# Kernel optimization log

Measured on AMD Instinct MI355X. Metric: run time of the kernel, lower is better.

## Reference

```python
import jax, jax.numpy as jnp
import numpy as np
import math

ROWS, COLS, N_NODES = 256, 1024, 500000


def setup_inputs() -> dict:
    key = jax.random.key(0)
    ks = jax.random.split(key, 16)
    stdv_row = 1.0 / math.sqrt(ROWS)
    u = lambda k, shape, s: jax.random.uniform(k, shape, jnp.float32, -s, s)
    return {
        "prev_Q": jax.random.normal(ks[0], (ROWS, COLS), jnp.float32),
        "prev_Z": jax.random.normal(ks[1], (N_NODES, ROWS), jnp.float32),
        "mask": jnp.zeros((N_NODES,), jnp.float32),
        "scorer": u(ks[2], (ROWS, 1), stdv_row),
        "W_u": u(ks[3], (ROWS, ROWS), stdv_row),
        "U_u": u(ks[4], (ROWS, ROWS), stdv_row),
        "b_u": jnp.zeros((ROWS, COLS), jnp.float32),
        "W_r": u(ks[5], (ROWS, ROWS), stdv_row),
        "U_r": u(ks[6], (ROWS, ROWS), stdv_row),
        "b_r": jnp.zeros((ROWS, COLS), jnp.float32),
        "W_h": u(ks[7], (ROWS, ROWS), stdv_row),
        "U_h": u(ks[8], (ROWS, ROWS), stdv_row),
        "b_h": jnp.zeros((ROWS, COLS), jnp.float32),
    }


def reference(prev_Q, prev_Z, mask, scorer, W_u, U_u, b_u, W_r, U_r, b_r, W_h, U_h, b_h):
    k = b_u.shape[1]  # cols == TopK k
    # --- TopK node selection (k <= num_nodes, no -inf masked scores) ---
    scores = (prev_Z @ scorer).ravel() / jnp.linalg.norm(scorer) + mask  # [N]
    vals, idx = jax.lax.top_k(scores, k)                                 # [k]
    # selected nodes scaled by tanh(score), then transposed -> [rows, k]
    z_topk = (prev_Z[idx] * jnp.tanh(vals)[:, None]).T
    # --- matrix GRU gates ---
    update = jax.nn.sigmoid(W_u @ z_topk + U_u @ prev_Q + b_u)
    reset = jax.nn.sigmoid(W_r @ z_topk + U_r @ prev_Q + b_r)
    h_cap = jax.nn.relu(W_h @ z_topk + U_h @ (reset * prev_Q) + b_h)
    new_Q = (1.0 - update) * prev_Q + update * h_cap
    return new_Q
```

## Files before the change

kernel.cpp:

```cpp
#include <hip/hip_runtime.h>
#include <hip/hip_bf16.h>

#define NN 500000

typedef short bf16x8 __attribute__((ext_vector_type(8)));
typedef float f32x4 __attribute__((ext_vector_type(4)));

__device__ __forceinline__ unsigned f2key(float f){
    unsigned u = __float_as_uint(f);
    return (u & 0x80000000u) ? ~u : (u | 0x80000000u);
}
__device__ __forceinline__ unsigned long long d2key(double d){
    unsigned long long u = (unsigned long long)__double_as_longlong(d);
    return (u & 0x8000000000000000ull) ? ~u : (u | 0x8000000000000000ull);
}
__device__ __forceinline__ double key2d(unsigned long long k){
    unsigned long long u = (k & 0x8000000000000000ull) ? (k & 0x7FFFFFFFFFFFFFFFull) : ~k;
    return __longlong_as_double((long long)u);
}
__device__ __forceinline__ float sigmoidf_(float x){
    return 1.0f / (1.0f + expf(-x));
}
__device__ __forceinline__ short f2bf(float x){
    __hip_bfloat16 h = __float2bfloat16(x);
    return *reinterpret_cast<short*>(&h);
}

__global__ __launch_bounds__(256) void score_kernel(
    const float4* __restrict__ Z4, const float* __restrict__ mask,
    const float* __restrict__ scorer, double* __restrict__ scores_d)
{
    __shared__ double nred[256];
    __shared__ double s_invn;
    int tid = threadIdx.x;
    {
        double v = (double)scorer[tid];
        nred[tid] = v * v;
        __syncthreads();
        for (int s = 128; s > 0; s >>= 1){
            if (tid < s) nred[tid] += nred[tid + s];
            __syncthreads();
        }
        if (tid == 0) s_invn = 1.0 / sqrt(nred[0]);
        __syncthreads();
    }
    double invn = s_invn;
    int sl = tid & 15;
    int grp = tid >> 4;
    int gid = blockIdx.x * 16 + grp;
    const float4* s4 = (const float4*)scorer;
    float4 s0 = s4[sl], s1 = s4[sl + 16], s2 = s4[sl + 32], s3 = s4[sl + 48];
    for (int r = gid; r < NN; r += 24576){
        const float4* zp = Z4 + (size_t)r * 64;
        float4 z0 = zp[sl], z1 = zp[sl + 16], z2 = zp[sl + 32], z3 = zp[sl + 48];
        double p0 = (double)z0.x * s0.x + (double)z0.y * s0.y + (double)z0.z * s0.z + (double)z0.w * s0.w;
        double p1 = (double)z1.x * s1.x + (double)z1.y * s1.y + (double)z1.z * s1.z + (double)z1.w * s1.w;
        double p2 = (double)z2.x * s2.x + (double)z2.y * s2.y + (double)z2.z * s2.z + (double)z2.w * s2.w;
        double p3 = (double)z3.x * s3.x + (double)z3.y * s3.y + (double)z3.z * s3.z + (double)z3.w * s3.w;
        double d = (p0 + p1) + (p2 + p3);
        d += __shfl_xor(d, 8, 16);
        d += __shfl_xor(d, 4, 16);
        d += __shfl_xor(d, 2, 16);
        d += __shfl_xor(d, 1, 16);
        if (sl == 0){
            scores_d[r] = d * invn + (double)mask[r];
        }
    }
}

__global__ __launch_bounds__(256) void hist_transpose_kernel(
    const double* __restrict__ scores_d, unsigned* __restrict__ hist,
    const float* __restrict__ prev_Q, float* __restrict__ Qt)
{
    __shared__ __attribute__((aligned(16))) char smem[16640];
    int tid = threadIdx.x;
    int b = blockIdx.x;
    if (b < 256){
        unsigned* h = (unsigned*)smem;
        for (int i = tid; i < 4096; i += 256) h[i] = 0u;
        __syncthreads();
        for (int i = b * 256 + tid; i < NN; i += 65536){
            double sd = scores_d[i];
            atomicAdd(&h[f2key((float)sd) >> 20], 1u);
        }
        __syncthreads();
        for (int i = tid; i < 4096; i += 256){
            unsigned c = h[i];
            if (c) atomicAdd(&hist[i], c);
        }
    } else {
        float (*tile)[65] = (float (*)[65])smem;
        int tb = b - 256;
        int n0 = (tb & 15) * 64, m0 = (tb >> 4) * 64;
        for (int rep = 0; rep < 16; ++rep){
            int lin = tid + rep * 256;
            int r = lin >> 6, c = lin & 63;
            tile[r][c] = prev_Q[(m0 + r) * 1024 + n0 + c];
        }
        __syncthreads();
        for (int rep = 0; rep < 16; ++rep){
            int lin = tid + rep * 256;
            int r = lin >> 6, c = lin & 63;
            Qt[(n0 + r) * 256 + m0 + c] = tile[c][r];
        }
    }
}

__global__ __launch_bounds__(256) void collect_kernel(
    const double* __restrict__ scores_d, const unsigned* __restrict__ hist,
    unsigned* __restrict__ meta,
    unsigned long long* __restrict__ ckey, unsigned* __restrict__ cidx)
{
    __shared__ unsigned hl[4096];
    __shared__ unsigned part[256];
    __shared__ unsigned s_thr;
    int tid = threadIdx.x;
    for (int i = tid; i < 4096; i += 256) hl[i] = hist[i];
    __syncthreads();
    int hi = 4096 - 16 * tid;
    unsigned s = 0;
    for (int bb = hi - 16; bb < hi; ++bb) s += hl[bb];
    part[tid] = s;
    __syncthreads();
    for (int off = 1; off < 256; off <<= 1){
        unsigned v = (tid >= off) ? part[tid - off] : 0u;
        __syncthreads();
        part[tid] += v;
        __syncthreads();
    }
    unsigned incl = part[tid];
    unsigned excl = incl - s;
    if (excl < 1024u && incl >= 1024u){
        unsigned c = excl;
        int bb;
        for (bb = hi - 1; bb >= hi - 16; --bb){
            c += hl[bb];
            if (c >= 1024u) break;
        }
        s_thr = ((unsigned)bb) << 20;
    }
    __syncthreads();
    unsigned thr = s_thr;
    int i = blockIdx.x * 256 + tid;
    if (i < NN){
        double sd = scores_d[i];
        if (f2key((float)sd) >= thr){
            unsigned p = atomicAdd(&meta[3], 1u);
            if (p < 4096u){ ckey[p] = d2key(sd); cidx[p] = (unsigned)i; }
        }
    }
}

__global__ __launch_bounds__(1024) void sort_emit_kernel(const unsigned long long* __restrict__ ckey,
                                                         const unsigned* __restrict__ cidx,
                                                         const unsigned* __restrict__ meta,
                                                         unsigned* __restrict__ sel_idx,
                                                         float* __restrict__ sel_t)
{
    __shared__ unsigned long long sk[4096];
    __shared__ unsigned si[4096];
    int t = threadIdx.x;
    unsigned n = meta[3];
    if (n > 4096u) n = 4096u;
    int m = 1024;
    while (m < (int)n) m <<= 1;
    for (int i = t; i < m; i += 1024){
        if (i < (int)n){ sk[i] = ckey[i]; si[i] = cidx[i]; }
        else           { sk[i] = 0ull;    si[i] = 0xFFFFFFFFu; }
    }
    __syncthreads();
    int m2 = m >> 1;
    for (int k = 2; k <= m; k <<= 1){
        for (int j = k >> 1; j > 0; j >>= 1){
            for (int p = t; p < m2; p += 1024){
                int i = ((p & ~(j - 1)) << 1) | (p & (j - 1));
                int ip = i | j;
                unsigned long long ka = sk[i], kb = sk[ip];
                unsigned ia = si[i], ib = si[ip];
                bool ab = (ka > kb) || (ka == kb && ia < ib);
                bool desc = ((i & k) == 0);
                bool sw = desc ? (!ab) : ab;
                if (sw){ sk[i] = kb; sk[ip] = ka; si[i] = ib; si[ip] = ia; }
            }
            __syncthreads();
        }
    }
    sel_idx[t] = si[t];
    sel_t[t] = tanhf((float)key2d(sk[t]));
}

__global__ void gather_kernel(const float4* __restrict__ Z4,
                              const unsigned* __restrict__ sel_idx,
                              const float* __restrict__ sel_t,
                              float4* __restrict__ Xc4)
{
    int lane = threadIdx.x & 63;
    int col = (blockIdx.x << 2) + (threadIdx.x >> 6);
    unsigned idx = sel_idx[col];
    float tv = sel_t[col];
    float4 z = Z4[(size_t)idx * 64 + lane];
    float4 o; o.x = z.x * tv; o.y = z.y * tv; o.z = z.z * tv; o.w = z.w * tv;
    Xc4[col * 64 + lane] = o;
}

__global__ __launch_bounds__(256) void gemm1_mfma(
    const float* __restrict__ Wu, const float* __restrict__ Uu, const float* __restrict__ bu,
    const float* __restrict__ Wr, const float* __restrict__ Ur, const float* __restrict__ br,
    const float* __restrict__ Wh, const float* __restrict__ bh,
    const float* __restrict__ Xc, const float* __restrict__ Qt, const float* __restrict__ Q,
    float* __restrict__ Umat, float* __restrict__ RQt, float* __restrict__ P3m)
{
    __shared__ short As[4096];
    __shared__ short Xs[4096];
    int g = blockIdx.z;
    int n0 = blockIdx.x * 64, m0 = blockIdx.y * 64;
    int tid = threadIdx.x;
    int l = tid & 63, w = tid >> 6;
    int q = l >> 4, c16 = l & 15;
    f32x4 acc[4];
    #pragma unroll
    for (int i = 0; i < 4; ++i) acc[i] = (f32x4){0.f, 0.f, 0.f, 0.f};
    const float* W0 = (g == 0) ? Wu : (g == 1) ? Wr : Wh;
    const float* W1 = (g == 0) ? Uu : (g == 1) ? Ur : Wh;
    int KMAX = (g == 2) ? 256 : 512;
    for (int k0 = 0; k0 < KMAX; k0 += 64){
        const float* Asrc = (k0 < 256) ? W0 : W1;
        const float* Xsrc = (k0 < 256) ? Xc : Qt;
        int koff = k0 & 255;
        #pragma unroll
        for (int i = 0; i < 4; ++i){
            int f = tid + (i << 8);
            int row = f >> 4, c = f & 15;
            float4 av = *(const float4*)&Asrc[(m0 + row) * 256 + koff + (c << 2)];
            float4 xv = *(const float4*)&Xsrc[(n0 + row) * 256 + koff + (c << 2)];
            int kb = (c << 3) ^ ((row & 7) << 4);
            short4 ah; ah.x = f2bf(av.x); ah.y = f2bf(av.y); ah.z = f2bf(av.z); ah.w = f2bf(av.w);
            short4 xh; xh.x = f2bf(xv.x); xh.y = f2bf(xv.y); xh.z = f2bf(xv.z); xh.w = f2bf(xv.w);
            *(short4*)((char*)As + row * 128 + kb) = ah;
            *(short4*)((char*)Xs + row * 128 + kb) = xh;
        }
        __syncthreads();
        int swz = (c16 & 7) << 4;
        bf16x8 a0 = *(const bf16x8*)((const char*)As + ((w << 4) + c16) * 128 + (((q << 4)     ) ^ swz));
        bf16x8 a1 = *(const bf16x8*)((const char*)As + ((w << 4) + c16) * 128 + ((64 + (q << 4)) ^ swz));
        #pragma unroll
        for (int nr = 0; nr < 4; ++nr){
            int xrow = (nr << 4) + c16;
            bf16x8 b0 = *(const bf16x8*)((const char*)Xs + xrow * 128 + (((q << 4)     ) ^ swz));
            bf16x8 b1 = *(const bf16x8*)((const char*)Xs + xrow * 128 + ((64 + (q << 4)) ^ swz));
            acc[nr] = __builtin_amdgcn_mfma_f32_16x16x32_bf16(a0, b0, acc[nr], 0, 0, 0);
            acc[nr] = __builtin_amdgcn_mfma_f32_16x16x32_bf16(a1, b1, acc[nr], 0, 0, 0);
        }
        __syncthreads();
    }
    int mrow = m0 + (w << 4) + (q << 2);
    if (g == 0){
        #pragma unroll
        for (int nr = 0; nr < 4; ++nr){
            int ncol = n0 + (nr << 4) + c16;
            #pragma unroll
            for (int r = 0; r < 4; ++r){
                int idx = (mrow + r) * 1024 + ncol;
                Umat[idx] = sigmoidf_(acc[nr][r] + bu[idx]);
            }
        }
    } else if (g == 1){
        #pragma unroll
        for (int nr = 0; nr < 4; ++nr){
            int ncol = n0 + (nr << 4) + c16;
            float4 o;
            float* op = (float*)&o;
            #pragma unroll
            for (int r = 0; r < 4; ++r){
                int idx = (mrow + r) * 1024 + ncol;
                op[r] = sigmoidf_(acc[nr][r] + br[idx]) * Q[idx];
            }
            *(float4*)&RQt[ncol * 256 + mrow] = o;
        }
    } else {
        #pragma unroll
        for (int nr = 0; nr < 4; ++nr){
            int ncol = n0 + (nr << 4) + c16;
            #pragma unroll
            for (int r = 0; r < 4; ++r){
                int idx = (mrow + r) * 1024 + ncol;
                P3m[idx] = acc[nr][r] + bh[idx];
            }
        }
    }
}

__global__ __launch_bounds__(256) void gemm2_mfma(
    const float* __restrict__ Uh, const float* __restrict__ RQt,
    const float* __restrict__ P3m, const float* __restrict__ Umat,
    const float* __restrict__ Q, float* __restrict__ out)
{
    __shared__ short As[4096];
    __shared__ short Xs[4096];
    int n0 = blockIdx.x * 64, m0 = blockIdx.y * 64;
    int tid = threadIdx.x;
    int l = tid & 63, w = tid >> 6;
    int q = l >> 4, c16 = l & 15;
    f32x4 acc[4];
    #pragma unroll
    for (int i = 0; i < 4; ++i) acc[i] = (f32x4){0.f, 0.f, 0.f, 0.f};
    for (int k0 = 0; k0 < 256; k0 += 64){
        #pragma unroll
        for (int i = 0; i < 4; ++i){
            int f = tid + (i << 8);
            int row = f >> 4, c = f & 15;
            float4 av = *(const float4*)&Uh[(m0 + row) * 256 + k0 + (c << 2)];
            float4 xv = *(const float4*)&RQt[(n0 + row) * 256 + k0 + (c << 2)];
            int kb = (c << 3) ^ ((row & 7) << 4);
            short4 ah; ah.x = f2bf(av.x); ah.y = f2bf(av.y); ah.z = f2bf(av.z); ah.w = f2bf(av.w);
            short4 xh; xh.x = f2bf(xv.x); xh.y = f2bf(xv.y); xh.z = f2bf(xv.z); xh.w = f2bf(xv.w);
            *(short4*)((char*)As + row * 128 + kb) = ah;
            *(short4*)((char*)Xs + row * 128 + kb) = xh;
        }
        __syncthreads();
        int swz = (c16 & 7) << 4;
        bf16x8 a0 = *(const bf16x8*)((const char*)As + ((w << 4) + c16) * 128 + (((q << 4)     ) ^ swz));
        bf16x8 a1 = *(const bf16x8*)((const char*)As + ((w << 4) + c16) * 128 + ((64 + (q << 4)) ^ swz));
        #pragma unroll
        for (int nr = 0; nr < 4; ++nr){
            int xrow = (nr << 4) + c16;
            bf16x8 b0 = *(const bf16x8*)((const char*)Xs + xrow * 128 + (((q << 4)     ) ^ swz));
            bf16x8 b1 = *(const bf16x8*)((const char*)Xs + xrow * 128 + ((64 + (q << 4)) ^ swz));
            acc[nr] = __builtin_amdgcn_mfma_f32_16x16x32_bf16(a0, b0, acc[nr], 0, 0, 0);
            acc[nr] = __builtin_amdgcn_mfma_f32_16x16x32_bf16(a1, b1, acc[nr], 0, 0, 0);
        }
        __syncthreads();
    }
    int mrow = m0 + (w << 4) + (q << 2);
    #pragma unroll
    for (int nr = 0; nr < 4; ++nr){
        int ncol = n0 + (nr << 4) + c16;
        #pragma unroll
        for (int r = 0; r < 4; ++r){
            int idx = (mrow + r) * 1024 + ncol;
            float h = fmaxf(acc[nr][r] + P3m[idx], 0.0f);
            float u = Umat[idx];
            float qv = Q[idx];
            out[idx] = (1.0f - u) * qv + u * h;
        }
    }
}

extern "C" void kernel_launch(void* const* d_in, const int* in_sizes, int n_in,
                              void* d_out, int out_size, void* d_ws, size_t ws_size,
                              hipStream_t stream)
{
    const float* prev_Q = (const float*)d_in[0];
    const float* prev_Z = (const float*)d_in[1];
    const float* mask   = (const float*)d_in[2];
    const float* scorer = (const float*)d_in[3];
    const float* W_u = (const float*)d_in[4];
    const float* U_u = (const float*)d_in[5];
    const float* b_u = (const float*)d_in[6];
    const float* W_r = (const float*)d_in[7];
    const float* U_r = (const float*)d_in[8];
    const float* b_r = (const float*)d_in[9];
    const float* W_h = (const float*)d_in[10];
    const float* U_h = (const float*)d_in[11];
    const float* b_h = (const float*)d_in[12];

    char* ws = (char*)d_ws;
    double*             scores_d = (double*)            (ws + 0);
    unsigned*           hist     = (unsigned*)          (ws + 4000256);
    unsigned*           meta     = (unsigned*)          (ws + 4016640);
    unsigned long long* ckey     = (unsigned long long*)(ws + 4016704);
    unsigned*           cidx     = (unsigned*)          (ws + 4049472);
    unsigned*           sel_idx  = (unsigned*)          (ws + 4065856);
    float*              sel_t    = (float*)             (ws + 4069952);
    float*              Xc       = (float*)             (ws + 4100096);
    float*              Qt       = (float*)             (ws + 5148672);
    float*              Umat     = (float*)             (ws + 6197248);
    float*              RQt      = (float*)             (ws + 7245824);
    float*              P3m      = (float*)             (ws + 8294400);

    hipMemsetAsync(ws + 4000256, 0, 16448, stream);

    hipLaunchKernelGGL(score_kernel, dim3(1536), dim3(256), 0, stream,
                       (const float4*)prev_Z, mask, scorer, scores_d);
    hipLaunchKernelGGL(hist_transpose_kernel, dim3(320), dim3(256), 0, stream,
                       scores_d, hist, prev_Q, Qt);
    hipLaunchKernelGGL(collect_kernel, dim3(1954), dim3(256), 0, stream,
                       scores_d, hist, meta, ckey, cidx);
    hipLaunchKernelGGL(sort_emit_kernel, dim3(1), dim3(1024), 0, stream,
                       ckey, cidx, meta, sel_idx, sel_t);
    hipLaunchKernelGGL(gather_kernel, dim3(256), dim3(256), 0, stream,
                       (const float4*)prev_Z, sel_idx, sel_t, (float4*)Xc);
    hipLaunchKernelGGL(gemm1_mfma, dim3(16, 4, 3), dim3(256), 0, stream,
                       W_u, U_u, b_u, W_r, U_r, b_r, W_h, b_h,
                       Xc, Qt, prev_Q, Umat, RQt, P3m);
    hipLaunchKernelGGL(gemm2_mfma, dim3(16, 4), dim3(256), 0, stream,
                       U_h, RQt, P3m, Umat, prev_Q, (float*)d_out);
}
```

Baseline: 199.0 us.

## Replace single-block bitonic sort with multi-block rank-by-counting selection

The single 1024-thread block that bitonic-sorted up to 4096 candidates is replaced by a rank kernel over 16 blocks. Each thread computes its candidate's rank by comparing against every other candidate in shared memory, then writes the candidate directly if its rank falls within the top 1024. This spreads the work across more compute units and avoids the many barrier-separated sort stages, at the cost of O(n^2) comparisons and each block redundantly loading all candidates into shared memory.

```diff
diff --git a/kernel.cpp b/kernel.cpp
--- a/kernel.cpp
+++ b/kernel.cpp
@@ -151,42 +151,41 @@
     }
 }
 
-__global__ __launch_bounds__(1024) void sort_emit_kernel(const unsigned long long* __restrict__ ckey,
-                                                         const unsigned* __restrict__ cidx,
-                                                         const unsigned* __restrict__ meta,
-                                                         unsigned* __restrict__ sel_idx,
-                                                         float* __restrict__ sel_t)
-{
-    __shared__ unsigned long long sk[4096];
-    __shared__ unsigned si[4096];
-    int t = threadIdx.x;
+__global__ __launch_bounds__(256) void rank_emit_kernel(
+    const unsigned long long* __restrict__ ckey, const unsigned* __restrict__ cidx,
+    const unsigned* __restrict__ meta,
+    unsigned* __restrict__ sel_idx, float* __restrict__ sel_t)
+{
+    __shared__ unsigned long long k_s[4096];
+    __shared__ unsigned i_s[4096];
     unsigned n = meta[3];
     if (n > 4096u) n = 4096u;
-    int m = 1024;
-    while (m < (int)n) m <<= 1;
-    for (int i = t; i < m; i += 1024){
-        if (i < (int)n){ sk[i] = ckey[i]; si[i] = cidx[i]; }
-        else           { sk[i] = 0ull;    si[i] = 0xFFFFFFFFu; }
-    }
+    unsigned base = blockIdx.x * 256;
+    if (base >= n) return;
+    int tid = threadIdx.x;
+    for (unsigned i = tid; i < n; i += 256){ k_s[i] = ckey[i]; i_s[i] = cidx[i]; }
     __syncthreads();
-    int m2 = m >> 1;
-    for (int k = 2; k <= m; k <<= 1){
-        for (int j = k >> 1; j > 0; j >>= 1){
-            for (int p = t; p < m2; p += 1024){
-                int i = ((p & ~(j - 1)) << 1) | (p & (j - 1));
-                int ip = i | j;
-                unsigned long long ka = sk[i], kb = sk[ip];
-                unsigned ia = si[i], ib = si[ip];
-                bool ab = (ka > kb) || (ka == kb && ia < ib);
-                bool desc = ((i & k) == 0);
-                bool sw = desc ? (!ab) : ab;
-                if (sw){ sk[i] = kb; sk[ip] = ka; si[i] = ib; si[ip] = ia; }
-            }
-            __syncthreads();
-        }
-    }
-    sel_idx[t] = si[t];
-    sel_t[t] = tanhf((float)key2d(sk[t]));
+    unsigned c = base + tid;
+    if (c < n){
+        unsigned long long ki = k_s[c];
+        unsigned ii = i_s[c];
+        unsigned rank = 0;
+        unsigned j = 0;
+        for (; j + 4 <= n; j += 4){
+            unsigned long long k0 = k_s[j], k1 = k_s[j+1], k2 = k_s[j+2], k3 = k_s[j+3];
+            unsigned i0 = i_s[j], i1 = i_s[j+1], i2 = i_s[j+2], i3 = i_s[j+3];
+            rank += (unsigned)((k0 > ki) | ((k0 == ki) & (i0 < ii)));
+            rank += (unsigned)((k1 > ki) | ((k1 == ki) & (i1 < ii)));
+            rank += (unsigned)((k2 > ki) | ((k2 == ki) & (i2 < ii)));
+            rank += (unsigned)((k3 > ki) | ((k3 == ki) & (i3 < ii)));
+        }
+        for (; j < n; ++j)
+            rank += (unsigned)((k_s[j] > ki) | ((k_s[j] == ki) & (i_s[j] < ii)));
+        if (rank < 1024u){
+            sel_idx[rank] = ii;
+            sel_t[rank] = tanhf((float)key2d(ki));
+        }
+    }
 }
 
 __global__ void gather_kernel(const float4* __restrict__ Z4,
@@ -386,7 +385,7 @@
                        scores_d, hist, prev_Q, Qt);
     hipLaunchKernelGGL(collect_kernel, dim3(1954), dim3(256), 0, stream,
                        scores_d, hist, meta, ckey, cidx);
-    hipLaunchKernelGGL(sort_emit_kernel, dim3(1), dim3(1024), 0, stream,
+    hipLaunchKernelGGL(rank_emit_kernel, dim3(16), dim3(256), 0, stream,
                        ckey, cidx, meta, sel_idx, sel_t);
     hipLaunchKernelGGL(gather_kernel, dim3(256), dim3(256), 0, stream,
                        (const float4*)prev_Z, sel_idx, sel_t, (float4*)Xc);
```

Result: slower. 219.3 us (+10.2%).
